# Optimization experiments

Measured on AMD Instinct MI355X. Metric: run time of the kernel, lower is better.

The kernel has to match this reference:

```python
import jax, jax.numpy as jnp
from jax import lax
import numpy as np

B, T, F = 4, 2048, 128
DM, L, STRIDE, KF = 512, 4, 4, 2
N, DC, E = 16, 4, 2
DI = E * DM          # 1024 inner dim
R = (DM + 15) // 16  # 32 dt_rank
K = KF * STRIDE      # 8 front conv kernel
EPS = 1e-5

def _ln(x, w, b):
    m = x.mean(-1, keepdims=True)
    v = ((x - m) ** 2).mean(-1, keepdims=True)
    return (x - m) / jnp.sqrt(v + EPS) * w + b

def _causal_dwconv(x, w, b):
    # x: (B,Ts,DI), w: (DI,DC) depthwise causal conv
    xc = x.transpose(0, 2, 1)
    y = lax.conv_general_dilated(xc, w[:, None, :], (1,), [(DC - 1, 0)],
                                 feature_group_count=w.shape[0])
    return (y + b[None, :, None]).transpose(0, 2, 1)

def _selective_scan(dt, A, Bm, Cm, u):
    # dt,u: (B,Ts,DI); A: (DI,N); Bm,Cm: (B,Ts,N)
    dA = jnp.exp(dt[..., None] * A)                  # (B,Ts,DI,N)
    dBu = (dt * u)[..., None] * Bm[:, :, None, :]    # (B,Ts,DI,N)
    def step(h, inp):
        dA_t, dBu_t, C_t = inp
        h = dA_t * h + dBu_t
        y = jnp.einsum('bdn,bn->bd', h, C_t)
        return h, y
    h0 = jnp.zeros((u.shape[0], DI, N), u.dtype)
    _, ys = lax.scan(step, h0, (dA.transpose(1, 0, 2, 3),
                                dBu.transpose(1, 0, 2, 3),
                                Cm.transpose(1, 0, 2)))
    return ys.transpose(1, 0, 2)

def _mamba(x, in_w, cw, cb, xp_w, dtp_w, dtp_b, A_log, Dp, out_w):
    xz = jnp.einsum('btd,ed->bte', x, in_w)          # (B,Ts,2*DI)
    xi, z = jnp.split(xz, 2, axis=-1)
    xi = jax.nn.silu(_causal_dwconv(xi, cw, cb))
    x_dbl = jnp.einsum('btd,ed->bte', xi, xp_w)      # (B,Ts,R+2N)
    dt, Bm, Cm = jnp.split(x_dbl, [R, R + N], axis=-1)
    dt = jax.nn.softplus(jnp.einsum('btr,dr->btd', dt, dtp_w) + dtp_b)
    y = _selective_scan(dt, -jnp.exp(A_log), Bm, Cm, xi)
    y = (y + xi * Dp) * jax.nn.silu(z)
    return jnp.einsum('btd,od->bto', y, out_w)

def _forward(x, conv_w, conv_b, in_proj_w, conv1d_w, conv1d_b, x_proj_w,
             dt_proj_w, dt_proj_b, A_log, D_skip, ln_w, ln_b, out_proj_w,
             norm_w, norm_b):
    T_orig = x.shape[1]
    # causal strided front conv: pad (K-1,0), stride=STRIDE, then GELU
    h = lax.conv_general_dilated(x.transpose(0, 2, 1), conv_w, (STRIDE,),
                                 [(K - 1, 0)])
    h = jax.nn.gelu((h + conv_b[None, :, None]).transpose(0, 2, 1),
                    approximate=False)               # (B,T//STRIDE,DM)
    for l in range(L):
        hn = _ln(h, ln_w[l], ln_b[l])
        h = h + _mamba(hn, in_proj_w[l], conv1d_w[l], conv1d_b[l],
                       x_proj_w[l], dt_proj_w[l], dt_proj_b[l],
                       A_log[l], D_skip[l], out_proj_w[l])
    h = _ln(h, norm_w, norm_b)
    # repeat_interleave upsample back to original resolution
    return jnp.repeat(h, STRIDE, axis=1)[:, :T_orig, :]

def setup_inputs():
    key = jax.random.key(0)
    ks = jax.random.split(key, 8)
    g = lambda i, shape, s=0.02: jax.random.normal(ks[i], shape, jnp.float32) * s
    A_log = jnp.tile(jnp.log(jnp.arange(1, N + 1, dtype=jnp.float32)), (L, DI, 1))
    return dict(
        x=jax.random.normal(ks[0], (B, T, F), jnp.float32),
        conv_w=g(1, (DM, F, K)), conv_b=jnp.zeros((DM,), jnp.float32),
        in_proj_w=g(2, (L, 2 * DI, DM)),
        conv1d_w=g(3, (L, DI, DC), 0.2),
        conv1d_b=jnp.zeros((L, DI), jnp.float32),
        x_proj_w=g(4, (L, R + 2 * N, DI)),
        dt_proj_w=g(5, (L, DI, R), 0.1),
        dt_proj_b=jnp.full((L, DI), -2.0, jnp.float32),
        A_log=A_log,
        D_skip=jnp.ones((L, DI), jnp.float32),
        ln_w=jnp.ones((L, DM), jnp.float32),
        ln_b=jnp.zeros((L, DM), jnp.float32),
        out_proj_w=g(6, (L, DM, DI)),
        norm_w=jnp.ones((DM,), jnp.float32),
        norm_b=jnp.zeros((DM,), jnp.float32),
    )

def reference(x, conv_w, conv_b, in_proj_w, conv1d_w, conv1d_b, x_proj_w,
              dt_proj_w, dt_proj_b, A_log, D_skip, ln_w, ln_b, out_proj_w,
              norm_w, norm_b):
    return _forward(x, conv_w, conv_b, in_proj_w, conv1d_w, conv1d_b, x_proj_w,
                    dt_proj_w, dt_proj_b, A_log, D_skip, ln_w, ln_b, out_proj_w,
                    norm_w, norm_b)
```

## Files before the change

### kernel.cpp

```cpp
#include <hip/hip_runtime.h>
#include <hip/hip_bf16.h>

typedef unsigned short u16;
typedef u16 u16x8 __attribute__((ext_vector_type(8)));
typedef __bf16 bf16x8 __attribute__((ext_vector_type(8)));
typedef float f32x4 __attribute__((ext_vector_type(4)));

#define GLOAD16(gsrc, ldst) \
  __builtin_amdgcn_global_load_lds((const __attribute__((address_space(1))) void*)(gsrc), \
                                   (__attribute__((address_space(3))) void*)(ldst), 16, 0, 0)

__device__ __forceinline__ u16 f2bf(float f) {
  union { float f; unsigned u; } c; c.f = f;
  unsigned r = c.u + 0x7FFFu + ((c.u >> 16) & 1u);
  return (u16)(r >> 16);
}
__device__ __forceinline__ float bf2f(u16 v) {
  union { unsigned u; float f; } c; c.u = ((unsigned)v) << 16;
  return c.f;
}

__global__ __launch_bounds__(256) void cast_weights_k(
    const float* __restrict__ in_w, const float* __restrict__ xp_w,
    const float* __restrict__ out_w, const float* __restrict__ conv_w,
    const float* __restrict__ A_log, const float* __restrict__ c1w,
    const float* __restrict__ x,
    u16* __restrict__ winb, u16* __restrict__ wxpb, u16* __restrict__ woutb,
    u16* __restrict__ wconvb, float* __restrict__ Apre, float* __restrict__ cwt,
    u16* __restrict__ xcolb) {
  int i = blockIdx.x * 256 + threadIdx.x;
  if (i < 1048576) {
    const float4 v = *(const float4*)(in_w + (size_t)i * 4);
    ushort2 lo = {f2bf(v.x), f2bf(v.y)}, hi = {f2bf(v.z), f2bf(v.w)};
    *(ushort2*)(winb + (size_t)i * 4) = lo;
    *(ushort2*)(winb + (size_t)i * 4 + 2) = hi;
    return;
  }
  i -= 1048576;
  if (i < 65536) {
    const float4 v = *(const float4*)(xp_w + (size_t)i * 4);
    ushort2 lo = {f2bf(v.x), f2bf(v.y)}, hi = {f2bf(v.z), f2bf(v.w)};
    *(ushort2*)(wxpb + (size_t)i * 4) = lo;
    *(ushort2*)(wxpb + (size_t)i * 4 + 2) = hi;
    return;
  }
  i -= 65536;
  if (i < 524288) {
    const float4 v = *(const float4*)(out_w + (size_t)i * 4);
    ushort2 lo = {f2bf(v.x), f2bf(v.y)}, hi = {f2bf(v.z), f2bf(v.w)};
    *(ushort2*)(woutb + (size_t)i * 4) = lo;
    *(ushort2*)(woutb + (size_t)i * 4 + 2) = hi;
    return;
  }
  i -= 524288;
  if (i < 131072) {
    const int m = i >> 8, r = (i & 255) * 4;
    const int kk = r >> 7, ff = r & 127;
    const float* src = conv_w + m * 1024 + kk;
    ushort2 lo = {f2bf(src[(ff + 0) * 8]), f2bf(src[(ff + 1) * 8])};
    ushort2 hi = {f2bf(src[(ff + 2) * 8]), f2bf(src[(ff + 3) * 8])};
    *(ushort2*)(wconvb + (size_t)i * 4) = lo;
    *(ushort2*)(wconvb + (size_t)i * 4 + 2) = hi;
    return;
  }
  i -= 131072;
  if (i < 16384) {
    const float4 v = *(const float4*)(A_log + (size_t)i * 4);
    float4 o;
    o.x = -__expf(v.x); o.y = -__expf(v.y); o.z = -__expf(v.z); o.w = -__expf(v.w);
    *(float4*)(Apre + (size_t)i * 4) = o;
    return;
  }
  i -= 16384;
  if (i < 4096) {
    const int og = i * 4, l = og >> 12, r = og & 4095;
    const int j = r >> 10, d0 = r & 1023;
    float4 o;
    o.x = c1w[l * 4096 + (d0 + 0) * 4 + j];
    o.y = c1w[l * 4096 + (d0 + 1) * 4 + j];
    o.z = c1w[l * 4096 + (d0 + 2) * 4 + j];
    o.w = c1w[l * 4096 + (d0 + 3) * 4 + j];
    *(float4*)(cwt + (size_t)i * 4) = o;
    return;
  }
  i -= 4096;
  if (i < 524288) {
    const int col = (i & 255) * 4, tok = i >> 8;
    const int kk = col >> 7, ff = col & 127;
    const int b = tok >> 9, to = tok & 511;
    const int t = to * 4 + kk - 7;
    float4 v = {0.f, 0.f, 0.f, 0.f};
    if (t >= 0) v = *(const float4*)(x + ((size_t)b * 2048 + t) * 128 + ff);
    ushort2 lo = {f2bf(v.x), f2bf(v.y)}, hi = {f2bf(v.z), f2bf(v.w)};
    *(ushort2*)(xcolb + (size_t)i * 4) = lo;
    *(ushort2*)(xcolb + (size_t)i * 4 + 2) = hi;
  }
}

template <int NW>
__global__ __launch_bounds__(NW * 64) void gemm2_k(
    const u16* __restrict__ A, int lda, const u16* __restrict__ Bw, int ldb,
    u16* __restrict__ C, int ldc, int Ks, size_t mn) {
  __shared__ __align__(16) char smem[NW * 16384];
  const int tid = threadIdx.x, lane = tid & 63, wid = tid >> 6;
  const int bm = blockIdx.x, bn = blockIdx.y;
  const int Kw = Ks / NW;
  const size_t koff = (size_t)blockIdx.z * Ks + (size_t)wid * Kw;
  char* base = smem + wid * 16384;
  const int srow = lane >> 2, sslot = lane & 3;
  const int nk = Kw >> 5;
  f32x4 acc[4][4] = {};

  auto stage = [&](int buf, int kt) {
#pragma unroll
    for (int c = 0; c < 8; ++c) {
      int lrow, gr, ldx; const u16* src;
      if (c < 4) { lrow = c * 16 + srow; gr = bm * 64 + lrow; src = A; ldx = lda; }
      else { lrow = (c - 4) * 16 + srow; gr = bn * 64 + lrow; src = Bw; ldx = ldb; }
      const int slot = sslot ^ ((lrow >> 1) & 3);
      GLOAD16(src + (size_t)gr * ldx + koff + kt * 32 + slot * 8,
              base + buf * 8192 + c * 1024);
    }
  };

  stage(0, 0);
  if (nk > 1) stage(1, 1);
  const int s = lane >> 4, r0 = lane & 15;
  for (int kt = 0; kt < nk; ++kt) {
    const int p = kt & 1;
    if (kt + 1 < nk) asm volatile("s_waitcnt vmcnt(8)" ::: "memory");
    else             asm volatile("s_waitcnt vmcnt(0)" ::: "memory");
    __builtin_amdgcn_sched_barrier(0);
    bf16x8 af[4], bfv[4];
#pragma unroll
    for (int i = 0; i < 4; ++i) {
      const int r = i * 16 + r0;
      af[i] = *(const bf16x8*)(base + p * 8192 + r * 64 + ((s ^ ((r >> 1) & 3)) << 4));
      bfv[i] = *(const bf16x8*)(base + p * 8192 + 4096 + r * 64 + ((s ^ ((r >> 1) & 3)) << 4));
    }
    asm volatile("s_waitcnt lgkmcnt(0)" ::: "memory");
    __builtin_amdgcn_sched_barrier(0);
    if (kt + 2 < nk) stage(p, kt + 2);
#pragma unroll
    for (int mi = 0; mi < 4; ++mi)
#pragma unroll
      for (int ni = 0; ni < 4; ++ni)
        acc[mi][ni] = __builtin_amdgcn_mfma_f32_16x16x32_bf16(af[mi], bfv[ni],
                                                              acc[mi][ni], 0, 0, 0);
    __builtin_amdgcn_sched_barrier(0);
  }
  if constexpr (NW == 2) {
    if (wid == 1) {
      f32x4* dst = (f32x4*)(smem + 16384);
#pragma unroll
      for (int mi = 0; mi < 4; ++mi)
#pragma unroll
        for (int ni = 0; ni < 4; ++ni)
          dst[(mi * 4 + ni) * 64 + lane] = acc[mi][ni];
    }
    __syncthreads();
    if (wid == 1) return;
    const f32x4* src1 = (const f32x4*)(smem + 16384);
#pragma unroll
    for (int mi = 0; mi < 4; ++mi)
#pragma unroll
      for (int ni = 0; ni < 4; ++ni)
        acc[mi][ni] += src1[(mi * 4 + ni) * 64 + lane];
  }
  const int er0 = lane & 15, eg4 = lane >> 4;
  u16* Cz = C + (size_t)blockIdx.z * mn;
#pragma unroll
  for (int mi = 0; mi < 4; ++mi)
#pragma unroll
    for (int ni = 0; ni < 4; ++ni) {
      const int col = bn * 64 + ni * 16 + er0;
#pragma unroll
      for (int r = 0; r < 4; ++r) {
        const int row = bm * 64 + mi * 16 + eg4 * 4 + r;
        Cz[(size_t)row * ldc + col] = f2bf(acc[mi][ni][r]);
      }
    }
}

template <int MODE>
__global__ __launch_bounds__(256) void red_ln_k(
    const u16* __restrict__ P, float* __restrict__ h,
    const float* __restrict__ bias, const float* __restrict__ w,
    const float* __restrict__ bb, u16* __restrict__ o, float* __restrict__ oup) {
  const int row = blockIdx.x * 4 + (threadIdx.x >> 6);
  const int lane = threadIdx.x & 63;
  const size_t base = (size_t)row * 512 + lane * 8;
  float v[8];
  if constexpr (MODE == 0) {
#pragma unroll
    for (int j = 0; j < 8; ++j) v[j] = 0.f;
  } else {
    float4 a = *(const float4*)(h + base);
    float4 b4 = *(const float4*)(h + base + 4);
    v[0] = a.x; v[1] = a.y; v[2] = a.z; v[3] = a.w;
    v[4] = b4.x; v[5] = b4.y; v[6] = b4.z; v[7] = b4.w;
  }
#pragma unroll
  for (int s2 = 0; s2 < 4; ++s2) {
    const u16x8 pv = *(const u16x8*)(P + (size_t)s2 * 1048576 + base);
#pragma unroll
    for (int j = 0; j < 8; ++j) v[j] += bf2f(pv[j]);
  }
  if constexpr (MODE == 0) {
    const int col = lane * 8;
#pragma unroll
    for (int j = 0; j < 8; ++j) {
      const float t = v[j] + bias[col + j];
      v[j] = 0.5f * t * (1.f + erff(t * 0.70710678118f));
    }
  }
  if constexpr (MODE != 2) {
    float4 oa; oa.x = v[0]; oa.y = v[1]; oa.z = v[2]; oa.w = v[3];
    float4 ob; ob.x = v[4]; ob.y = v[5]; ob.z = v[6]; ob.w = v[7];
    *(float4*)(h + base) = oa;
    *(float4*)(h + base + 4) = ob;
  }
  float s = 0.f, sq = 0.f;
#pragma unroll
  for (int j = 0; j < 8; ++j) { s += v[j]; sq += v[j] * v[j]; }
  for (int off = 32; off; off >>= 1) { s += __shfl_xor(s, off); sq += __shfl_xor(sq, off); }
  const float m = s * (1.f / 512.f);
  const float rs = rsqrtf(sq * (1.f / 512.f) - m * m + 1e-5f);
  const float* wp = w + lane * 8; const float* bp = bb + lane * 8;
  float nv[8];
#pragma unroll
  for (int j = 0; j < 8; ++j) nv[j] = (v[j] - m) * rs * wp[j] + bp[j];
  if constexpr (MODE != 2) {
    uint4 uu;
    uu.x = (unsigned)f2bf(nv[0]) | ((unsigned)f2bf(nv[1]) << 16);
    uu.y = (unsigned)f2bf(nv[2]) | ((unsigned)f2bf(nv[3]) << 16);
    uu.z = (unsigned)f2bf(nv[4]) | ((unsigned)f2bf(nv[5]) << 16);
    uu.w = (unsigned)f2bf(nv[6]) | ((unsigned)f2bf(nv[7]) << 16);
    *(uint4*)(o + base) = uu;
  } else {
    const int bi = row >> 9, t0 = row & 511;
    float4 lo; lo.x = nv[0]; lo.y = nv[1]; lo.z = nv[2]; lo.w = nv[3];
    float4 hi; hi.x = nv[4]; hi.y = nv[5]; hi.z = nv[6]; hi.w = nv[7];
    float* obp = oup + ((size_t)bi * 2048 + (size_t)t0 * 4) * 512 + lane * 8;
#pragma unroll
    for (int q = 0; q < 4; ++q) {
      *(float4*)(obp + (size_t)q * 512) = lo;
      *(float4*)(obp + (size_t)q * 512 + 4) = hi;
    }
  }
}

__global__ __launch_bounds__(256) void redxdt_k(
    const u16* __restrict__ ppB, const float* __restrict__ dtw,
    const float* __restrict__ dtbias, float* __restrict__ xdbl,
    u16* __restrict__ dtbb) {
  __shared__ float xls[32 * 64];
  const int tid = threadIdx.x;
  const int tg = blockIdx.x >> 2, dblk = blockIdx.x & 3;
  const int T0 = tg * 32;
  for (int i = tid; i < 2048; i += 256) {
    const size_t off = (size_t)T0 * 64 + i;
    float v = 0.f;
#pragma unroll
    for (int s2 = 0; s2 < 8; ++s2) v += bf2f(ppB[(size_t)s2 * 131072 + off]);
    xls[i] = v;
    if (dblk == 0) xdbl[off] = v;
  }
  const int d = dblk * 256 + tid;
  float4 w[8];
#pragma unroll
  for (int j = 0; j < 8; ++j) w[j] = *(const float4*)(dtw + (size_t)d * 32 + j * 4);
  const float b = dtbias[d];
  __syncthreads();
  for (int t = 0; t < 32; ++t) {
    const float4* xr = (const float4*)&xls[t * 64];
    float acc = b;
#pragma unroll
    for (int j = 0; j < 8; ++j) {
      const float4 xv = xr[j];
      acc = fmaf(w[j].x, xv.x, acc); acc = fmaf(w[j].y, xv.y, acc);
      acc = fmaf(w[j].z, xv.z, acc); acc = fmaf(w[j].w, xv.w, acc);
    }
    dtbb[(size_t)(T0 + t) * 1024 + d] =
        f2bf(fmaxf(acc, 0.f) + __logf(1.f + __expf(-fabsf(acc))));
  }
}

__global__ __launch_bounds__(256) void dwconv_k(const u16* __restrict__ xzb,
                                                const float* __restrict__ cwt,
                                                const float* __restrict__ cb,
                                                u16* __restrict__ xib) {
  const int i = blockIdx.x * 256 + threadIdx.x;
  const int d0 = (i & 127) * 8, tok = i >> 7, t = tok & 511;
  const u16* p = xzb + (size_t)tok * 2048 + d0;
  const float4 b0 = *(const float4*)(cb + d0);
  const float4 b1 = *(const float4*)(cb + d0 + 4);
  float acc[8] = {b0.x, b0.y, b0.z, b0.w, b1.x, b1.y, b1.z, b1.w};
#pragma unroll
  for (int j = 0; j < 4; ++j) {
    const int ts = t + j - 3;
    if (ts >= 0) {
      const u16x8 xv = *(const u16x8*)(p + (j - 3) * 2048);
      const float4 wa = *(const float4*)(cwt + j * 1024 + d0);
      const float4 wb = *(const float4*)(cwt + j * 1024 + d0 + 4);
      acc[0] = fmaf(bf2f(xv[0]), wa.x, acc[0]);
      acc[1] = fmaf(bf2f(xv[1]), wa.y, acc[1]);
      acc[2] = fmaf(bf2f(xv[2]), wa.z, acc[2]);
      acc[3] = fmaf(bf2f(xv[3]), wa.w, acc[3]);
      acc[4] = fmaf(bf2f(xv[4]), wb.x, acc[4]);
      acc[5] = fmaf(bf2f(xv[5]), wb.y, acc[5]);
      acc[6] = fmaf(bf2f(xv[6]), wb.z, acc[6]);
      acc[7] = fmaf(bf2f(xv[7]), wb.w, acc[7]);
    }
  }
  u16x8 o;
#pragma unroll
  for (int e = 0; e < 8; ++e)
    o[e] = f2bf(acc[e] / (1.f + __expf(-acc[e])));
  *(u16x8*)(xib + (size_t)i * 8) = o;
}

__global__ __launch_bounds__(256) void scan1_k(const u16* __restrict__ dtbb,
                                               const u16* __restrict__ xib,
                                               const float* __restrict__ xd,
                                               const float* __restrict__ Ap,
                                               unsigned* __restrict__ hA) {
  const int blk = blockIdx.x;
  const int d = (blk & 3) * 256 + threadIdx.x;
  const int c = (blk >> 2) & 31, b = blk >> 7;
  float A[16], h[16], ap[16];
#pragma unroll
  for (int n = 0; n < 16; ++n) { A[n] = Ap[d * 16 + n]; h[n] = 0.f; ap[n] = 1.f; }
  const int t0 = c * 16;
  for (int t = t0; t < t0 + 16; ++t) {
    const int tok = b * 512 + t;
    const float dtv = bf2f(dtbb[(size_t)tok * 1024 + d]);
    const float u = bf2f(xib[(size_t)tok * 1024 + d]);
    const float s = dtv * u;
    const float* Bp = xd + (size_t)tok * 64 + 32;
#pragma unroll
    for (int n = 0; n < 16; ++n) {
      const float dA = __expf(dtv * A[n]);
      h[n] = dA * h[n] + s * Bp[n];
      ap[n] *= dA;
    }
  }
#pragma unroll
  for (int n = 0; n < 16; ++n) {
    const size_t o = ((size_t)(b * 32 + c) * 16 + n) * 1024 + d;
    hA[o] = (unsigned)f2bf(h[n]) | ((unsigned)f2bf(ap[n]) << 16);
  }
}

__global__ __launch_bounds__(256) void scan2_k(const unsigned* __restrict__ hA,
                                               u16* __restrict__ hI) {
  const int bi = blockIdx.x >> 6;
  const int n = (blockIdx.x >> 2) & 15;
  const int d = (blockIdx.x & 3) * 256 + threadIdx.x;
  float h = 0.f;
  for (int c = 0; c < 32; ++c) {
    const size_t o = ((size_t)((bi * 32 + c) * 16 + n)) * 1024 + d;
    hI[o] = f2bf(h);
    const unsigned pk = hA[o];
    h = fmaf(bf2f((u16)(pk >> 16)), h, bf2f((u16)(pk & 0xffffu)));
  }
}

__global__ __launch_bounds__(256) void scan3_k(const u16* __restrict__ dtbb,
                                               const u16* __restrict__ xib,
                                               const float* __restrict__ xd,
                                               const float* __restrict__ Ap,
                                               const u16* __restrict__ hI,
                                               const u16* __restrict__ xzb,
                                               const float* __restrict__ Dp,
                                               u16* __restrict__ y2b) {
  const int blk = blockIdx.x;
  const int d = (blk & 3) * 256 + threadIdx.x;
  const int c = (blk >> 2) & 31, b = blk >> 7;
  float A[16], h[16];
#pragma unroll
  for (int n = 0; n < 16; ++n) {
    A[n] = Ap[d * 16 + n];
    h[n] = bf2f(hI[((size_t)(b * 32 + c) * 16 + n) * 1024 + d]);
  }
  const float Dd = Dp[d];
  const int t0 = c * 16;
  for (int t = t0; t < t0 + 16; ++t) {
    const int tok = b * 512 + t;
    const float dtv = bf2f(dtbb[(size_t)tok * 1024 + d]);
    const float u = bf2f(xib[(size_t)tok * 1024 + d]);
    const float s = dtv * u;
    const float* Bp = xd + (size_t)tok * 64 + 32;
    const float* Cp = xd + (size_t)tok * 64 + 48;
    float y = 0.f;
#pragma unroll
    for (int n = 0; n < 16; ++n) {
      const float dA = __expf(dtv * A[n]);
      h[n] = dA * h[n] + s * Bp[n];
      y = fmaf(h[n], Cp[n], y);
    }
    const float z = bf2f(xzb[(size_t)tok * 2048 + 1024 + d]);
    const float sz = z / (1.f + __expf(-z));
    y2b[(size_t)tok * 1024 + d] = f2bf((y + u * Dd) * sz);
  }
}

extern "C" void kernel_launch(void* const* d_in, const int* in_sizes, int n_in,
                              void* d_out, int out_size, void* d_ws, size_t ws_size,
                              hipStream_t stream) {
  const float* x      = (const float*)d_in[0];
  const float* conv_w = (const float*)d_in[1];
  const float* conv_b = (const float*)d_in[2];
  const float* in_w   = (const float*)d_in[3];
  const float* c1w    = (const float*)d_in[4];
  const float* c1b    = (const float*)d_in[5];
  const float* xp_w   = (const float*)d_in[6];
  const float* dt_w   = (const float*)d_in[7];
  const float* dt_b   = (const float*)d_in[8];
  const float* A_log  = (const float*)d_in[9];
  const float* D_skip = (const float*)d_in[10];
  const float* ln_w   = (const float*)d_in[11];
  const float* ln_b   = (const float*)d_in[12];
  const float* out_w  = (const float*)d_in[13];
  const float* norm_w = (const float*)d_in[14];
  const float* norm_b = (const float*)d_in[15];
  float* out = (float*)d_out;

  float* f = (float*)d_ws;
  float* h    = f; f += 1048576;
  float* xdbl = f; f += 131072;
  float* Apre = f; f += 65536;
  float* cwt  = f; f += 16384;
  unsigned* hA = (unsigned*)f; f += 2097152;
  u16* ub = (u16*)f;
  u16* hnb    = ub; ub += 1048576;
  u16* xzb    = ub; ub += 4194304;
  u16* xib    = ub; ub += 2097152;
  u16* dtbb   = ub; ub += 2097152;
  u16* y2b    = ub; ub += 2097152;
  u16* xcolb  = ub; ub += 2097152;
  u16* hIu    = ub; ub += 2097152;
  u16* pp     = ub; ub += 4194304;
  u16* ppB    = ub; ub += 1048576;
  u16* winb   = ub; ub += 4194304;
  u16* wxpb   = ub; ub += 262144;
  u16* woutb  = ub; ub += 2097152;
  u16* wconvb = ub; ub += 524288;

  cast_weights_k<<<9040, 256, 0, stream>>>(in_w, xp_w, out_w, conv_w, A_log, c1w,
                                           x, winb, wxpb, woutb, wconvb, Apre,
                                           cwt, xcolb);
  gemm2_k<2><<<dim3(32, 8, 4), 128, 0, stream>>>(xcolb, 1024, wconvb, 1024,
                                                 pp, 512, 256, (size_t)1048576);
  red_ln_k<0><<<512, 256, 0, stream>>>(pp, h, conv_b, ln_w, ln_b, hnb, nullptr);
  for (int l = 0; l < 4; ++l) {
    gemm2_k<2><<<dim3(32, 32, 1), 128, 0, stream>>>(hnb, 512, winb + l * 1048576,
                                                    512, xzb, 2048, 512, 0);
    dwconv_k<<<1024, 256, 0, stream>>>(xzb, cwt + l * 4096, c1b + l * 1024, xib);
    gemm2_k<2><<<dim3(32, 1, 8), 128, 0, stream>>>(xib, 1024, wxpb + l * 65536,
                                                   1024, ppB, 64, 128, (size_t)131072);
    redxdt_k<<<256, 256, 0, stream>>>(ppB, dt_w + l * 32768, dt_b + l * 1024,
                                      xdbl, dtbb);
    scan1_k<<<512, 256, 0, stream>>>(dtbb, xib, xdbl, Apre + l * 16384, hA);
    scan2_k<<<256, 256, 0, stream>>>(hA, hIu);
    scan3_k<<<512, 256, 0, stream>>>(dtbb, xib, xdbl, Apre + l * 16384, hIu, xzb,
                                     D_skip + l * 1024, y2b);
    gemm2_k<2><<<dim3(32, 8, 4), 128, 0, stream>>>(y2b, 1024, woutb + l * 524288,
                                                   1024, pp, 512, 256, (size_t)1048576);
    if (l < 3) {
      red_ln_k<1><<<512, 256, 0, stream>>>(pp, h, nullptr, ln_w + (l + 1) * 512,
                                           ln_b + (l + 1) * 512, hnb, nullptr);
    } else {
      red_ln_k<2><<<512, 256, 0, stream>>>(pp, h, nullptr, norm_w, norm_b,
                                           nullptr, out);
    }
  }
}
```

Measured before the change: 346.0 us.

## Fuse split-K reduction and dt projection into both scan passes

Removes the separate redxdt kernel. Each scan chunk block now reduces the split-K x_proj partials for its 16 tokens into shared memory and computes dt = softplus(dt_proj) on the fly in both scan1 and scan3. This drops one launch per layer and the round trips of the bf16 dt buffer and the fp32 x_dbl buffer through memory, at the cost of doing the reduction and dt GEMV twice. scan2 is also changed to issue all 32 chunk loads before its serial combine and to write results afterwards, which exposes memory-level parallelism.

```diff
diff --git a/kernel.cpp b/kernel.cpp
--- a/kernel.cpp
+++ b/kernel.cpp
@@ -250,42 +250,6 @@
   }
 }
 
-__global__ __launch_bounds__(256) void redxdt_k(
-    const u16* __restrict__ ppB, const float* __restrict__ dtw,
-    const float* __restrict__ dtbias, float* __restrict__ xdbl,
-    u16* __restrict__ dtbb) {
-  __shared__ float xls[32 * 64];
-  const int tid = threadIdx.x;
-  const int tg = blockIdx.x >> 2, dblk = blockIdx.x & 3;
-  const int T0 = tg * 32;
-  for (int i = tid; i < 2048; i += 256) {
-    const size_t off = (size_t)T0 * 64 + i;
-    float v = 0.f;
-#pragma unroll
-    for (int s2 = 0; s2 < 8; ++s2) v += bf2f(ppB[(size_t)s2 * 131072 + off]);
-    xls[i] = v;
-    if (dblk == 0) xdbl[off] = v;
-  }
-  const int d = dblk * 256 + tid;
-  float4 w[8];
-#pragma unroll
-  for (int j = 0; j < 8; ++j) w[j] = *(const float4*)(dtw + (size_t)d * 32 + j * 4);
-  const float b = dtbias[d];
-  __syncthreads();
-  for (int t = 0; t < 32; ++t) {
-    const float4* xr = (const float4*)&xls[t * 64];
-    float acc = b;
-#pragma unroll
-    for (int j = 0; j < 8; ++j) {
-      const float4 xv = xr[j];
-      acc = fmaf(w[j].x, xv.x, acc); acc = fmaf(w[j].y, xv.y, acc);
-      acc = fmaf(w[j].z, xv.z, acc); acc = fmaf(w[j].w, xv.w, acc);
-    }
-    dtbb[(size_t)(T0 + t) * 1024 + d] =
-        f2bf(fmaxf(acc, 0.f) + __logf(1.f + __expf(-fabsf(acc))));
-  }
-}
-
 __global__ __launch_bounds__(256) void dwconv_k(const u16* __restrict__ xzb,
                                                 const float* __restrict__ cwt,
                                                 const float* __restrict__ cb,
@@ -320,28 +284,47 @@
   *(u16x8*)(xib + (size_t)i * 8) = o;
 }
 
-__global__ __launch_bounds__(256) void scan1_k(const u16* __restrict__ dtbb,
-                                               const u16* __restrict__ xib,
-                                               const float* __restrict__ xd,
-                                               const float* __restrict__ Ap,
-                                               unsigned* __restrict__ hA) {
+__global__ __launch_bounds__(256) void scan1_k(
+    const u16* __restrict__ ppB, const float* __restrict__ dtw,
+    const float* __restrict__ dtbias, const u16* __restrict__ xib,
+    const float* __restrict__ Ap, unsigned* __restrict__ hA) {
+  __shared__ float xls[16 * 64];
   const int blk = blockIdx.x;
-  const int d = (blk & 3) * 256 + threadIdx.x;
+  const int tid = threadIdx.x;
+  const int d = (blk & 3) * 256 + tid;
   const int c = (blk >> 2) & 31, b = blk >> 7;
+  const int T0 = b * 512 + c * 16;
+  for (int i = tid; i < 1024; i += 256) {
+    const size_t off = (size_t)T0 * 64 + i;
+    float v = 0.f;
+#pragma unroll
+    for (int s2 = 0; s2 < 8; ++s2) v += bf2f(ppB[(size_t)s2 * 131072 + off]);
+    xls[i] = v;
+  }
+  float4 w[8];
+#pragma unroll
+  for (int j = 0; j < 8; ++j) w[j] = *(const float4*)(dtw + (size_t)d * 32 + j * 4);
+  const float bia = dtbias[d];
   float A[16], h[16], ap[16];
 #pragma unroll
   for (int n = 0; n < 16; ++n) { A[n] = Ap[d * 16 + n]; h[n] = 0.f; ap[n] = 1.f; }
-  const int t0 = c * 16;
-  for (int t = t0; t < t0 + 16; ++t) {
-    const int tok = b * 512 + t;
-    const float dtv = bf2f(dtbb[(size_t)tok * 1024 + d]);
-    const float u = bf2f(xib[(size_t)tok * 1024 + d]);
-    const float s = dtv * u;
-    const float* Bp = xd + (size_t)tok * 64 + 32;
+  __syncthreads();
+  for (int t = 0; t < 16; ++t) {
+    const float* xr = &xls[t * 64];
+    float acc = bia;
+#pragma unroll
+    for (int j = 0; j < 8; ++j) {
+      const float4 xv = ((const float4*)xr)[j];
+      acc = fmaf(w[j].x, xv.x, acc); acc = fmaf(w[j].y, xv.y, acc);
+      acc = fmaf(w[j].z, xv.z, acc); acc = fmaf(w[j].w, xv.w, acc);
+    }
+    const float dt = fmaxf(acc, 0.f) + __logf(1.f + __expf(-fabsf(acc)));
+    const float u = bf2f(xib[(size_t)(T0 + t) * 1024 + d]);
+    const float s = dt * u;
 #pragma unroll
     for (int n = 0; n < 16; ++n) {
-      const float dA = __expf(dtv * A[n]);
-      h[n] = dA * h[n] + s * Bp[n];
+      const float dA = __expf(dt * A[n]);
+      h[n] = dA * h[n] + s * xr[32 + n];
       ap[n] *= dA;
     }
   }
@@ -357,26 +340,44 @@
   const int bi = blockIdx.x >> 6;
   const int n = (blockIdx.x >> 2) & 15;
   const int d = (blockIdx.x & 3) * 256 + threadIdx.x;
+  const size_t base = ((size_t)(bi * 32) * 16 + n) * 1024 + d;
+  unsigned pk[32];
+#pragma unroll
+  for (int c = 0; c < 32; ++c) pk[c] = hA[base + (size_t)c * 16384];
   float h = 0.f;
+  u16 outv[32];
+#pragma unroll
   for (int c = 0; c < 32; ++c) {
-    const size_t o = ((size_t)((bi * 32 + c) * 16 + n)) * 1024 + d;
-    hI[o] = f2bf(h);
-    const unsigned pk = hA[o];
-    h = fmaf(bf2f((u16)(pk >> 16)), h, bf2f((u16)(pk & 0xffffu)));
-  }
-}
-
-__global__ __launch_bounds__(256) void scan3_k(const u16* __restrict__ dtbb,
-                                               const u16* __restrict__ xib,
-                                               const float* __restrict__ xd,
-                                               const float* __restrict__ Ap,
-                                               const u16* __restrict__ hI,
-                                               const u16* __restrict__ xzb,
-                                               const float* __restrict__ Dp,
-                                               u16* __restrict__ y2b) {
+    outv[c] = f2bf(h);
+    h = fmaf(bf2f((u16)(pk[c] >> 16)), h, bf2f((u16)(pk[c] & 0xffffu)));
+  }
+#pragma unroll
+  for (int c = 0; c < 32; ++c) hI[base + (size_t)c * 16384] = outv[c];
+}
+
+__global__ __launch_bounds__(256) void scan3_k(
+    const u16* __restrict__ ppB, const float* __restrict__ dtw,
+    const float* __restrict__ dtbias, const u16* __restrict__ xib,
+    const float* __restrict__ Ap, const u16* __restrict__ hI,
+    const u16* __restrict__ xzb, const float* __restrict__ Dp,
+    u16* __restrict__ y2b) {
+  __shared__ float xls[16 * 64];
   const int blk = blockIdx.x;
-  const int d = (blk & 3) * 256 + threadIdx.x;
+  const int tid = threadIdx.x;
+  const int d = (blk & 3) * 256 + tid;
   const int c = (blk >> 2) & 31, b = blk >> 7;
+  const int T0 = b * 512 + c * 16;
+  for (int i = tid; i < 1024; i += 256) {
+    const size_t off = (size_t)T0 * 64 + i;
+    float v = 0.f;
+#pragma unroll
+    for (int s2 = 0; s2 < 8; ++s2) v += bf2f(ppB[(size_t)s2 * 131072 + off]);
+    xls[i] = v;
+  }
+  float4 w[8];
+#pragma unroll
+  for (int j = 0; j < 8; ++j) w[j] = *(const float4*)(dtw + (size_t)d * 32 + j * 4);
+  const float bia = dtbias[d];
   float A[16], h[16];
 #pragma unroll
   for (int n = 0; n < 16; ++n) {
@@ -384,20 +385,26 @@
     h[n] = bf2f(hI[((size_t)(b * 32 + c) * 16 + n) * 1024 + d]);
   }
   const float Dd = Dp[d];
-  const int t0 = c * 16;
-  for (int t = t0; t < t0 + 16; ++t) {
-    const int tok = b * 512 + t;
-    const float dtv = bf2f(dtbb[(size_t)tok * 1024 + d]);
+  __syncthreads();
+  for (int t = 0; t < 16; ++t) {
+    const float* xr = &xls[t * 64];
+    float acc = bia;
+#pragma unroll
+    for (int j = 0; j < 8; ++j) {
+      const float4 xv = ((const float4*)xr)[j];
+      acc = fmaf(w[j].x, xv.x, acc); acc = fmaf(w[j].y, xv.y, acc);
+      acc = fmaf(w[j].z, xv.z, acc); acc = fmaf(w[j].w, xv.w, acc);
+    }
+    const float dt = fmaxf(acc, 0.f) + __logf(1.f + __expf(-fabsf(acc)));
+    const int tok = T0 + t;
     const float u = bf2f(xib[(size_t)tok * 1024 + d]);
-    const float s = dtv * u;
-    const float* Bp = xd + (size_t)tok * 64 + 32;
-    const float* Cp = xd + (size_t)tok * 64 + 48;
+    const float s = dt * u;
     float y = 0.f;
 #pragma unroll
     for (int n = 0; n < 16; ++n) {
-      const float dA = __expf(dtv * A[n]);
-      h[n] = dA * h[n] + s * Bp[n];
-      y = fmaf(h[n], Cp[n], y);
+      const float dA = __expf(dt * A[n]);
+      h[n] = dA * h[n] + s * xr[32 + n];
+      y = fmaf(h[n], xr[48 + n], y);
     }
     const float z = bf2f(xzb[(size_t)tok * 2048 + 1024 + d]);
     const float sz = z / (1.f + __expf(-z));
@@ -428,7 +435,6 @@
 
   float* f = (float*)d_ws;
   float* h    = f; f += 1048576;
-  float* xdbl = f; f += 131072;
   float* Apre = f; f += 65536;
   float* cwt  = f; f += 16384;
   unsigned* hA = (unsigned*)f; f += 2097152;
@@ -436,7 +442,6 @@
   u16* hnb    = ub; ub += 1048576;
   u16* xzb    = ub; ub += 4194304;
   u16* xib    = ub; ub += 2097152;
-  u16* dtbb   = ub; ub += 2097152;
   u16* y2b    = ub; ub += 2097152;
   u16* xcolb  = ub; ub += 2097152;
   u16* hIu    = ub; ub += 2097152;
@@ -459,11 +464,11 @@
     dwconv_k<<<1024, 256, 0, stream>>>(xzb, cwt + l * 4096, c1b + l * 1024, xib);
     gemm2_k<2><<<dim3(32, 1, 8), 128, 0, stream>>>(xib, 1024, wxpb + l * 65536,
                                                    1024, ppB, 64, 128, (size_t)131072);
-    redxdt_k<<<256, 256, 0, stream>>>(ppB, dt_w + l * 32768, dt_b + l * 1024,
-                                      xdbl, dtbb);
-    scan1_k<<<512, 256, 0, stream>>>(dtbb, xib, xdbl, Apre + l * 16384, hA);
+    scan1_k<<<512, 256, 0, stream>>>(ppB, dt_w + l * 32768, dt_b + l * 1024,
+                                     xib, Apre + l * 16384, hA);
     scan2_k<<<256, 256, 0, stream>>>(hA, hIu);
-    scan3_k<<<512, 256, 0, stream>>>(dtbb, xib, xdbl, Apre + l * 16384, hIu, xzb,
+    scan3_k<<<512, 256, 0, stream>>>(ppB, dt_w + l * 32768, dt_b + l * 1024,
+                                     xib, Apre + l * 16384, hIu, xzb,
                                      D_skip + l * 1024, y2b);
     gemm2_k<2><<<dim3(32, 8, 4), 128, 0, stream>>>(y2b, 1024, woutb + l * 524288,
                                                    1024, pp, 512, 256, (size_t)1048576);
```

Result: faster. 324.1 us (-6.3%).
